# Kernel optimization log

Hardware: AMD Instinct MI355X
Metric: run time of the kernel (lower is better)

The kernel has to match this reference:

```python
import jax, jax.numpy as jnp
import numpy as np

B, N = 4096, 1024


def setup_inputs() -> dict:
    key = jax.random.key(0)
    k1, k2 = jax.random.split(key)
    cors = 0.1 * jax.random.normal(k1, (B, N, 3), dtype=jnp.float32)  # predicted correspondences/offsets
    p_src = jax.random.normal(k2, (B, N, 3), dtype=jnp.float32)       # source point cloud
    return {"cors": cors, "p_src": p_src}


def reference(cors, p_src):
    # p_pred = p_src + cors  (target points implied by correspondences)
    p_pred = p_src + cors
    # centroids over the point dimension: [B, 1, 3]
    src_centroid = jnp.mean(p_src, axis=1, keepdims=True)
    pred_centroid = jnp.mean(p_pred, axis=1, keepdims=True)
    src_trans = p_src - src_centroid
    pred_trans = p_pred - pred_centroid
    # 3x3 cross-covariance per batch: h = src_trans^T @ pred_trans  -> [B, 3, 3]
    h = jnp.einsum('bnd,bne->bde', src_trans, pred_trans)
    # tf.linalg.svd returns s, u, v with h = u diag(s) v^T; jnp returns u, s, vh with vh = v^T
    u, s, vh = jnp.linalg.svd(h, full_matrices=False)
    # r_est = v @ u^T = (u @ vh)^T
    r_est = jnp.swapaxes(jnp.matmul(u, vh), -1, -2)  # [B, 3, 3]
    # t_est = -r_est @ src_centroid^T + pred_centroid^T  -> [B, 3, 1]
    t_est = -jnp.matmul(r_est, jnp.swapaxes(src_centroid, -1, -2)) + jnp.swapaxes(pred_centroid, -1, -2)
    g_top = jnp.concatenate([r_est, t_est], axis=2)  # [B, 3, 4]
    last_row = jnp.broadcast_to(
        jnp.array([[[0.0, 0.0, 0.0, 1.0]]], dtype=g_top.dtype), (g_top.shape[0], 1, 4)
    )
    return jnp.concatenate([g_top, last_row], axis=1)  # [B, 4, 4]
```

## Files before the change

### kernel.cpp

```cpp
#include <hip/hip_runtime.h>


constexpr int NPTS    = 1024;
constexpr int THREADS = 256;
constexpr int NF4     = NPTS * 3 / 4;
constexpr int BPB     = 2;

__device__ __forceinline__ float dpp_qxor1(float x) {
    int y = __builtin_amdgcn_update_dpp(0, __float_as_int(x), 0xB1, 0xF, 0xF, true);
    return __int_as_float(y);
}
__device__ __forceinline__ float dpp_qxor2(float x) {
    int y = __builtin_amdgcn_update_dpp(0, __float_as_int(x), 0x4E, 0xF, 0xF, true);
    return __int_as_float(y);
}

__global__ __launch_bounds__(THREADS) void svd_layer_kernel(
    const float* __restrict__ cors,
    const float* __restrict__ p_src,
    float* __restrict__ out)
{
    __shared__ float4 lds_s[NF4];
    __shared__ float4 lds_c[NF4];
    __shared__ float  allS[BPB][4][16];

    const int t = threadIdx.x;
    const int wave = t >> 6, lane = t & 63;
    const int b0 = blockIdx.x * BPB;

    const float4* s4 = reinterpret_cast<const float4*>(p_src) + (size_t)b0 * NF4;
    const float4* c4 = reinterpret_cast<const float4*>(cors)  + (size_t)b0 * NF4;

    float4 a0 = s4[t], a1 = s4[t + 256], a2 = s4[t + 512];
    float4 d0 = c4[t], d1 = c4[t + 256], d2 = c4[t + 512];

    for (int k = 0; k < BPB; ++k) {
        lds_s[t] = a0; lds_s[t + 256] = a1; lds_s[t + 512] = a2;
        lds_c[t] = d0; lds_c[t + 256] = d1; lds_c[t + 512] = d2;
        __syncthreads();

        if (k + 1 < BPB) {
            const float4* sn = s4 + (size_t)(k + 1) * NF4;
            const float4* cn = c4 + (size_t)(k + 1) * NF4;
            a0 = sn[t]; a1 = sn[t + 256]; a2 = sn[t + 512];
            d0 = cn[t]; d1 = cn[t + 256]; d2 = cn[t + 512];
        }

        const float4 t0 = lds_s[t*3+0], t1 = lds_s[t*3+1], t2 = lds_s[t*3+2];
        const float4 u0 = lds_c[t*3+0], u1 = lds_c[t*3+1], u2 = lds_c[t*3+2];
        __syncthreads();

        const float sx[4] = {t0.x, t0.w, t1.z, t2.y};
        const float sy[4] = {t0.y, t1.x, t1.w, t2.z};
        const float sz[4] = {t0.z, t1.y, t2.x, t2.w};
        const float px[4] = {sx[0]+u0.x, sx[1]+u0.w, sx[2]+u1.z, sx[3]+u2.y};
        const float py[4] = {sy[0]+u0.y, sy[1]+u1.x, sy[2]+u1.w, sy[3]+u2.z};
        const float pz[4] = {sz[0]+u0.z, sz[1]+u1.y, sz[2]+u2.x, sz[3]+u2.w};

        float acc[15];
        #pragma unroll
        for (int i = 0; i < 15; ++i) acc[i] = 0.f;
        #pragma unroll
        for (int q = 0; q < 4; ++q) {
            acc[0]  += sx[q]; acc[1]  += sy[q]; acc[2]  += sz[q];
            acc[3]  += px[q]; acc[4]  += py[q]; acc[5]  += pz[q];
            acc[6]  += sx[q]*px[q]; acc[7]  += sx[q]*py[q]; acc[8]  += sx[q]*pz[q];
            acc[9]  += sy[q]*px[q]; acc[10] += sy[q]*py[q]; acc[11] += sy[q]*pz[q];
            acc[12] += sz[q]*px[q]; acc[13] += sz[q]*py[q]; acc[14] += sz[q]*pz[q];
        }

        #pragma unroll
        for (int i = 0; i < 15; ++i) acc[i] += dpp_qxor1(acc[i]);
        #pragma unroll
        for (int i = 0; i < 15; ++i) acc[i] += dpp_qxor2(acc[i]);

        const int c = lane & 3;
        float r0 = (c==0)?acc[0]:(c==1)?acc[4]:(c==2)?acc[8] :acc[12];
        float r1 = (c==0)?acc[1]:(c==1)?acc[5]:(c==2)?acc[9] :acc[13];
        float r2 = (c==0)?acc[2]:(c==1)?acc[6]:(c==2)?acc[10]:acc[14];
        float r3 = (c==0)?acc[3]:(c==1)?acc[7]:(c==2)?acc[11]:0.f;

        #pragma unroll
        for (int off = 4; off <= 32; off <<= 1) {
            r0 += __shfl_xor(r0, off, 64);
            r1 += __shfl_xor(r1, off, 64);
            r2 += __shfl_xor(r2, off, 64);
            r3 += __shfl_xor(r3, off, 64);
        }

        if (lane < 4) {
            float* dst = &allS[k][wave][lane * 4];
            dst[0] = r0; dst[1] = r1; dst[2] = r2; dst[3] = r3;
        }
    }

    __syncthreads();
    if (t >= BPB) return;

    float S[15];
    #pragma unroll
    for (int i = 0; i < 15; ++i)
        S[i] = allS[t][0][i] + allS[t][1][i] + allS[t][2][i] + allS[t][3][i];

    const float invN = 1.0f / (float)NPTS;
    const float cs[3] = {S[0]*invN, S[1]*invN, S[2]*invN};
    const float cp[3] = {S[3]*invN, S[4]*invN, S[5]*invN};

    float Hm[3][3];
    #pragma unroll
    for (int i = 0; i < 3; ++i)
        #pragma unroll
        for (int j = 0; j < 3; ++j)
            Hm[i][j] = S[6 + i*3 + j] - (float)NPTS * cs[i] * cp[j];

    float K[3][3];
    #pragma unroll
    for (int i = 0; i < 3; ++i)
        #pragma unroll
        for (int j = 0; j < 3; ++j)
            K[i][j] = Hm[0][i]*Hm[0][j] + Hm[1][i]*Hm[1][j] + Hm[2][i]*Hm[2][j];

    const float tr3 = (K[0][0] + K[1][1] + K[2][2]) * (1.0f/3.0f);
    const float is  = 1.0f / fmaxf(tr3, 1e-30f);

    float Y[3][3], Z[3][3];
    #pragma unroll
    for (int i = 0; i < 3; ++i)
        #pragma unroll
        for (int j = 0; j < 3; ++j) {
            Y[i][j] = K[i][j] * is;
            Z[i][j] = (i == j) ? 1.0f : 0.0f;
        }

    #pragma unroll
    for (int it = 0; it < 6; ++it) {
        float W[3][3];
        #pragma unroll
        for (int i = 0; i < 3; ++i)
            #pragma unroll
            for (int j = 0; j < 3; ++j) {
                float w = Z[i][0]*Y[0][j] + Z[i][1]*Y[1][j] + Z[i][2]*Y[2][j];
                W[i][j] = ((i == j) ? 1.5f : 0.0f) - 0.5f * w;
            }
        float Yn[3][3], Zn[3][3];
        #pragma unroll
        for (int i = 0; i < 3; ++i)
            #pragma unroll
            for (int j = 0; j < 3; ++j) {
                Yn[i][j] = Y[i][0]*W[0][j] + Y[i][1]*W[1][j] + Y[i][2]*W[2][j];
                Zn[i][j] = W[i][0]*Z[0][j] + W[i][1]*Z[1][j] + W[i][2]*Z[2][j];
            }
        #pragma unroll
        for (int i = 0; i < 3; ++i)
            #pragma unroll
            for (int j = 0; j < 3; ++j) { Y[i][j] = Yn[i][j]; Z[i][j] = Zn[i][j]; }
    }

    const float rs = rsqrtf(fmaxf(tr3, 1e-30f));
    float R[3][3];
    #pragma unroll
    for (int i = 0; i < 3; ++i)
        #pragma unroll
        for (int j = 0; j < 3; ++j)
            R[i][j] = (Z[i][0]*Hm[j][0] + Z[i][1]*Hm[j][1] + Z[i][2]*Hm[j][2]) * rs;

    const float tx = cp[0] - (R[0][0]*cs[0] + R[0][1]*cs[1] + R[0][2]*cs[2]);
    const float ty = cp[1] - (R[1][0]*cs[0] + R[1][1]*cs[1] + R[1][2]*cs[2]);
    const float tz = cp[2] - (R[2][0]*cs[0] + R[2][1]*cs[1] + R[2][2]*cs[2]);

    float4* o4 = reinterpret_cast<float4*>(out + (size_t)(b0 + t) * 16);
    o4[0] = make_float4(R[0][0], R[0][1], R[0][2], tx);
    o4[1] = make_float4(R[1][0], R[1][1], R[1][2], ty);
    o4[2] = make_float4(R[2][0], R[2][1], R[2][2], tz);
    o4[3] = make_float4(0.f, 0.f, 0.f, 1.f);
}

extern "C" void kernel_launch(void* const* d_in, const int* in_sizes, int n_in,
                              void* d_out, int out_size, void* d_ws, size_t ws_size,
                              hipStream_t stream)
{
    const float* cors  = (const float*)d_in[0];
    const float* p_src = (const float*)d_in[1];
    float* out = (float*)d_out;
    const int B = in_sizes[0] / (NPTS * 3);
    const int grid = B / BPB;
    hipLaunchKernelGGL(svd_layer_kernel, dim3(grid), dim3(THREADS), 0, stream,
                       cors, p_src, out);
}
```

Measured before the change: 116.5 us.

## Load points directly as 12-byte structs, one batch per block without LDS

Replaces the coalesced float4 load plus LDS transpose with direct per-thread loads of 3-float structs, so each thread reads points t, t+256, t+512 and t+768 straight from global memory. It also drops the two-batch-per-block software pipelining and launches one block per batch. This removes LDS traffic and barriers, and the smaller shared-memory footprint allows more blocks per CU. In exchange, the 12-byte strided loads are less well vectorized and prefetching of the next batch is lost.

```diff
diff --git a/kernel.cpp b/kernel.cpp
--- a/kernel.cpp
+++ b/kernel.cpp
@@ -3,8 +3,8 @@
 
 constexpr int NPTS    = 1024;
 constexpr int THREADS = 256;
-constexpr int NF4     = NPTS * 3 / 4;
-constexpr int BPB     = 2;
+
+struct F3 { float x, y, z; };
 
 __device__ __forceinline__ float dpp_qxor1(float x) {
     int y = __builtin_amdgcn_update_dpp(0, __float_as_int(x), 0xB1, 0xF, 0xF, true);
@@ -20,87 +20,68 @@
     const float* __restrict__ p_src,
     float* __restrict__ out)
 {
-    __shared__ float4 lds_s[NF4];
-    __shared__ float4 lds_c[NF4];
-    __shared__ float  allS[BPB][4][16];
+    __shared__ float allS[4][16];
 
+    const int b = blockIdx.x;
     const int t = threadIdx.x;
     const int wave = t >> 6, lane = t & 63;
-    const int b0 = blockIdx.x * BPB;
+    const size_t base = (size_t)b * NPTS * 3;
 
-    const float4* s4 = reinterpret_cast<const float4*>(p_src) + (size_t)b0 * NF4;
-    const float4* c4 = reinterpret_cast<const float4*>(cors)  + (size_t)b0 * NF4;
+    const F3* sp = reinterpret_cast<const F3*>(p_src + base);
+    const F3* cq = reinterpret_cast<const F3*>(cors  + base);
 
-    float4 a0 = s4[t], a1 = s4[t + 256], a2 = s4[t + 512];
-    float4 d0 = c4[t], d1 = c4[t + 256], d2 = c4[t + 512];
+    const F3 s0 = sp[t], s1 = sp[t + 256], s2 = sp[t + 512], s3 = sp[t + 768];
+    const F3 c0 = cq[t], c1 = cq[t + 256], c2 = cq[t + 512], c3 = cq[t + 768];
 
-    for (int k = 0; k < BPB; ++k) {
-        lds_s[t] = a0; lds_s[t + 256] = a1; lds_s[t + 512] = a2;
-        lds_c[t] = d0; lds_c[t + 256] = d1; lds_c[t + 512] = d2;
-        __syncthreads();
+    const float sx[4] = {s0.x, s1.x, s2.x, s3.x};
+    const float sy[4] = {s0.y, s1.y, s2.y, s3.y};
+    const float sz[4] = {s0.z, s1.z, s2.z, s3.z};
+    const float px[4] = {s0.x + c0.x, s1.x + c1.x, s2.x + c2.x, s3.x + c3.x};
+    const float py[4] = {s0.y + c0.y, s1.y + c1.y, s2.y + c2.y, s3.y + c3.y};
+    const float pz[4] = {s0.z + c0.z, s1.z + c1.z, s2.z + c2.z, s3.z + c3.z};
 
-        if (k + 1 < BPB) {
-            const float4* sn = s4 + (size_t)(k + 1) * NF4;
-            const float4* cn = c4 + (size_t)(k + 1) * NF4;
-            a0 = sn[t]; a1 = sn[t + 256]; a2 = sn[t + 512];
-            d0 = cn[t]; d1 = cn[t + 256]; d2 = cn[t + 512];
-        }
-
-        const float4 t0 = lds_s[t*3+0], t1 = lds_s[t*3+1], t2 = lds_s[t*3+2];
-        const float4 u0 = lds_c[t*3+0], u1 = lds_c[t*3+1], u2 = lds_c[t*3+2];
-        __syncthreads();
-
-        const float sx[4] = {t0.x, t0.w, t1.z, t2.y};
-        const float sy[4] = {t0.y, t1.x, t1.w, t2.z};
-        const float sz[4] = {t0.z, t1.y, t2.x, t2.w};
-        const float px[4] = {sx[0]+u0.x, sx[1]+u0.w, sx[2]+u1.z, sx[3]+u2.y};
-        const float py[4] = {sy[0]+u0.y, sy[1]+u1.x, sy[2]+u1.w, sy[3]+u2.z};
-        const float pz[4] = {sz[0]+u0.z, sz[1]+u1.y, sz[2]+u2.x, sz[3]+u2.w};
-
-        float acc[15];
-        #pragma unroll
-        for (int i = 0; i < 15; ++i) acc[i] = 0.f;
-        #pragma unroll
-        for (int q = 0; q < 4; ++q) {
-            acc[0]  += sx[q]; acc[1]  += sy[q]; acc[2]  += sz[q];
-            acc[3]  += px[q]; acc[4]  += py[q]; acc[5]  += pz[q];
-            acc[6]  += sx[q]*px[q]; acc[7]  += sx[q]*py[q]; acc[8]  += sx[q]*pz[q];
-            acc[9]  += sy[q]*px[q]; acc[10] += sy[q]*py[q]; acc[11] += sy[q]*pz[q];
-            acc[12] += sz[q]*px[q]; acc[13] += sz[q]*py[q]; acc[14] += sz[q]*pz[q];
-        }
-
-        #pragma unroll
-        for (int i = 0; i < 15; ++i) acc[i] += dpp_qxor1(acc[i]);
-        #pragma unroll
-        for (int i = 0; i < 15; ++i) acc[i] += dpp_qxor2(acc[i]);
-
-        const int c = lane & 3;
-        float r0 = (c==0)?acc[0]:(c==1)?acc[4]:(c==2)?acc[8] :acc[12];
-        float r1 = (c==0)?acc[1]:(c==1)?acc[5]:(c==2)?acc[9] :acc[13];
-        float r2 = (c==0)?acc[2]:(c==1)?acc[6]:(c==2)?acc[10]:acc[14];
-        float r3 = (c==0)?acc[3]:(c==1)?acc[7]:(c==2)?acc[11]:0.f;
-
-        #pragma unroll
-        for (int off = 4; off <= 32; off <<= 1) {
-            r0 += __shfl_xor(r0, off, 64);
-            r1 += __shfl_xor(r1, off, 64);
-            r2 += __shfl_xor(r2, off, 64);
-            r3 += __shfl_xor(r3, off, 64);
-        }
-
-        if (lane < 4) {
-            float* dst = &allS[k][wave][lane * 4];
-            dst[0] = r0; dst[1] = r1; dst[2] = r2; dst[3] = r3;
-        }
+    float acc[15];
+    #pragma unroll
+    for (int i = 0; i < 15; ++i) acc[i] = 0.f;
+    #pragma unroll
+    for (int q = 0; q < 4; ++q) {
+        acc[0]  += sx[q]; acc[1]  += sy[q]; acc[2]  += sz[q];
+        acc[3]  += px[q]; acc[4]  += py[q]; acc[5]  += pz[q];
+        acc[6]  += sx[q]*px[q]; acc[7]  += sx[q]*py[q]; acc[8]  += sx[q]*pz[q];
+        acc[9]  += sy[q]*px[q]; acc[10] += sy[q]*py[q]; acc[11] += sy[q]*pz[q];
+        acc[12] += sz[q]*px[q]; acc[13] += sz[q]*py[q]; acc[14] += sz[q]*pz[q];
     }
 
+    #pragma unroll
+    for (int i = 0; i < 15; ++i) acc[i] += dpp_qxor1(acc[i]);
+    #pragma unroll
+    for (int i = 0; i < 15; ++i) acc[i] += dpp_qxor2(acc[i]);
+
+    const int c = lane & 3;
+    float r0 = (c==0)?acc[0]:(c==1)?acc[4]:(c==2)?acc[8] :acc[12];
+    float r1 = (c==0)?acc[1]:(c==1)?acc[5]:(c==2)?acc[9] :acc[13];
+    float r2 = (c==0)?acc[2]:(c==1)?acc[6]:(c==2)?acc[10]:acc[14];
+    float r3 = (c==0)?acc[3]:(c==1)?acc[7]:(c==2)?acc[11]:0.f;
+
+    #pragma unroll
+    for (int off = 4; off <= 32; off <<= 1) {
+        r0 += __shfl_xor(r0, off, 64);
+        r1 += __shfl_xor(r1, off, 64);
+        r2 += __shfl_xor(r2, off, 64);
+        r3 += __shfl_xor(r3, off, 64);
+    }
+
+    if (lane < 4) {
+        float* dst = &allS[wave][lane * 4];
+        dst[0] = r0; dst[1] = r1; dst[2] = r2; dst[3] = r3;
+    }
     __syncthreads();
-    if (t >= BPB) return;
+    if (t != 0) return;
 
     float S[15];
     #pragma unroll
     for (int i = 0; i < 15; ++i)
-        S[i] = allS[t][0][i] + allS[t][1][i] + allS[t][2][i] + allS[t][3][i];
+        S[i] = allS[0][i] + allS[1][i] + allS[2][i] + allS[3][i];
 
     const float invN = 1.0f / (float)NPTS;
     const float cs[3] = {S[0]*invN, S[1]*invN, S[2]*invN};
@@ -168,7 +149,7 @@
     const float ty = cp[1] - (R[1][0]*cs[0] + R[1][1]*cs[1] + R[1][2]*cs[2]);
     const float tz = cp[2] - (R[2][0]*cs[0] + R[2][1]*cs[1] + R[2][2]*cs[2]);
 
-    float4* o4 = reinterpret_cast<float4*>(out + (size_t)(b0 + t) * 16);
+    float4* o4 = reinterpret_cast<float4*>(out + (size_t)b * 16);
     o4[0] = make_float4(R[0][0], R[0][1], R[0][2], tx);
     o4[1] = make_float4(R[1][0], R[1][1], R[1][2], ty);
     o4[2] = make_float4(R[2][0], R[2][1], R[2][2], tz);
@@ -183,7 +164,6 @@
     const float* p_src = (const float*)d_in[1];
     float* out = (float*)d_out;
     const int B = in_sizes[0] / (NPTS * 3);
-    const int grid = B / BPB;
-    hipLaunchKernelGGL(svd_layer_kernel, dim3(grid), dim3(THREADS), 0, stream,
+    hipLaunchKernelGGL(svd_layer_kernel, dim3(B), dim3(THREADS), 0, stream,
                        cors, p_src, out);
 }
```

Measured after the change: 115.2 us. No clear change (-1.1%).
